# Kernel optimization log

Hardware: AMD Instinct MI355X
Metric: run time of the kernel (lower is better)

## Reference

```python
import jax, jax.numpy as jnp
import numpy as np

TEMP = 0.1
DX = 64  # feature dim of x; W1 rows [0:DX] multiply x, rows [DX:] multiply y


def setup_inputs() -> dict:
    key = jax.random.key(0)
    k1, k2, k3, k4 = jax.random.split(key, 4)
    n, d, hidden = 1024, 64, 256
    x = jax.random.normal(k1, (n, d), dtype=jnp.float32)
    y = jax.random.normal(k2, (n, d), dtype=jnp.float32)
    W1 = jax.random.normal(k3, (2 * d, hidden), dtype=jnp.float32) * (1.0 / np.sqrt(2 * d))
    b1 = jnp.zeros((hidden,), dtype=jnp.float32)
    w2 = jax.random.normal(k4, (hidden,), dtype=jnp.float32) * (1.0 / np.sqrt(hidden))
    b2 = jnp.zeros((), dtype=jnp.float32)
    return {"x": x, "y": y, "W1": W1, "b1": b1, "w2": w2, "b2": b2}


def reference(x, y, W1, b1, w2, b2):
    n = y.shape[0]
    W1x, W1y = W1[:DX], W1[DX:]
    xp = x @ W1x                      # [n, hidden], indexed by j (x_tile[i,j] = x[j])
    yp = y @ W1y                      # [n, hidden], indexed by i (y_tile[i,j] = y[i])
    # Positive pairs: scorer(cat(x_i, y_i))
    pos = (jax.nn.relu(xp + yp + b1) @ w2 + b2) / TEMP          # [n]
    h = jax.nn.relu(yp[:, None, :] + xp[None, :, :] + b1)        # [n, n, hidden]
    scores = (h @ w2 + b2) / TEMP                                 # [n, n]
    lse = jax.nn.logsumexp(scores, axis=1)                        # [n]
    lower_bound = pos.mean() - (lse.mean() - jnp.log(jnp.float32(n)))
    return -lower_bound
```

## Files before the change

### kernel.cpp

```cpp
#include <hip/hip_runtime.h>
#include <math.h>

#define NN 1024
#define DD 64
#define HH 256
#define TEMP_INV 10.0f
#define KCH 64
#define NCH (HH / KCH)


__global__ __launch_bounds__(256)
void k1_proj(const float* __restrict__ x, const float* __restrict__ y,
             const float* __restrict__ W1, const float* __restrict__ b1,
             float* __restrict__ xpbT, float* __restrict__ ypT)
{
    const int tid = threadIdx.x;
    const int i0 = blockIdx.x * 2;
    float ax0 = 0.f, ax1 = 0.f, ay0 = 0.f, ay1 = 0.f;
    #pragma unroll 8
    for (int kk = 0; kk < DD; ++kk) {
        const float wx = W1[kk * HH + tid];
        const float wy = W1[(DD + kk) * HH + tid];
        ax0 = fmaf(x[i0 * DD + kk],       wx, ax0);
        ax1 = fmaf(x[(i0 + 1) * DD + kk], wx, ax1);
        ay0 = fmaf(y[i0 * DD + kk],       wy, ay0);
        ay1 = fmaf(y[(i0 + 1) * DD + kk], wy, ay1);
    }
    const float b1t = b1[tid];
    *(float2*)&xpbT[tid * NN + i0] = make_float2(ax0 + b1t, ax1 + b1t);
    *(float2*)&ypT[tid * NN + i0]  = make_float2(ay0, ay1);
}

__global__ __launch_bounds__(512)
void k2_scores(const float* __restrict__ xpbT, const float* __restrict__ ypT,
               const float* __restrict__ w2, const float* __restrict__ b2,
               float* __restrict__ pmax, float* __restrict__ psum,
               float* __restrict__ pos)
{
    __shared__ float ys[2][KCH][64];
    __shared__ float xs[2][KCH][64];
    __shared__ float w2s[HH];
    const int t  = threadIdx.x;
    const int bj = blockIdx.x, bi = blockIdx.y;
    const int i0 = bi * 64, j0 = bj * 64;
    const int rr = t >> 5;
    const int cc = t & 31;

    if (t < HH) w2s[t] = w2[t];

    #define STAGE(c, buf)                                                      \
    {                                                                          \
        const int k0s = (c) * KCH;                                             \
        _Pragma("unroll")                                                      \
        for (int h = 0; h < 2; ++h) {                                          \
            const int f  = t + h * 512;                                        \
            const int r  = f >> 4;                                             \
            const int c4 = (f & 15) * 4;                                       \
            *(float4*)&ys[buf][r][c4] =                                        \
                *(const float4*)&ypT[(k0s + r) * NN + i0 + c4];                \
            *(float4*)&xs[buf][r][c4] =                                        \
                *(const float4*)&xpbT[(k0s + r) * NN + j0 + c4];               \
        }                                                                      \
    }

    float a00=0.f,a01=0.f, a10=0.f,a11=0.f, a20=0.f,a21=0.f, a30=0.f,a31=0.f;

    STAGE(0, 0);
    __syncthreads();
    for (int c = 0; c < NCH; ++c) {
        if (c + 1 < NCH) STAGE(c + 1, (c + 1) & 1);
        const int k0 = c * KCH;
        const int cur = c & 1;
        #pragma unroll 8
        for (int kk = 0; kk < KCH; ++kk) {
            const float w2k = w2s[k0 + kk];
            const float4 yv = *(const float4*)&ys[cur][kk][rr * 4];
            const float2 xv = *(const float2*)&xs[cur][kk][cc * 2];
            a00 = fmaf(fmaxf(yv.x + xv.x, 0.f), w2k, a00);
            a01 = fmaf(fmaxf(yv.x + xv.y, 0.f), w2k, a01);
            a10 = fmaf(fmaxf(yv.y + xv.x, 0.f), w2k, a10);
            a11 = fmaf(fmaxf(yv.y + xv.y, 0.f), w2k, a11);
            a20 = fmaf(fmaxf(yv.z + xv.x, 0.f), w2k, a20);
            a21 = fmaf(fmaxf(yv.z + xv.y, 0.f), w2k, a21);
            a30 = fmaf(fmaxf(yv.w + xv.x, 0.f), w2k, a30);
            a31 = fmaf(fmaxf(yv.w + xv.y, 0.f), w2k, a31);
        }
        __syncthreads();
    }
    #undef STAGE

    const float bb = b2[0];
    float s[4][2];
    s[0][0] = (a00 + bb) * TEMP_INV; s[0][1] = (a01 + bb) * TEMP_INV;
    s[1][0] = (a10 + bb) * TEMP_INV; s[1][1] = (a11 + bb) * TEMP_INV;
    s[2][0] = (a20 + bb) * TEMP_INV; s[2][1] = (a21 + bb) * TEMP_INV;
    s[3][0] = (a30 + bb) * TEMP_INV; s[3][1] = (a31 + bb) * TEMP_INV;

    if (bi == bj) {
        #pragma unroll
        for (int p = 0; p < 4; ++p)
            #pragma unroll
            for (int q = 0; q < 2; ++q)
                if (rr * 4 + p == cc * 2 + q)
                    pos[i0 + rr * 4 + p] = s[p][q];
    }

    float m[4], e[4];
    #pragma unroll
    for (int p = 0; p < 4; ++p) {
        m[p] = fmaxf(s[p][0], s[p][1]);
        e[p] = __expf(s[p][0] - m[p]) + __expf(s[p][1] - m[p]);
    }
    #pragma unroll
    for (int mk = 16; mk >= 1; mk >>= 1) {
        #pragma unroll
        for (int p = 0; p < 4; ++p) {
            const float mo = __shfl_xor(m[p], mk);
            const float eo = __shfl_xor(e[p], mk);
            const float mn = fmaxf(m[p], mo);
            e[p] = e[p] * __expf(m[p] - mn) + eo * __expf(mo - mn);
            m[p] = mn;
        }
    }
    if (cc == 0) {
        #pragma unroll
        for (int p = 0; p < 4; ++p) {
            const int row = i0 + rr * 4 + p;
            pmax[bj * NN + row] = m[p];
            psum[bj * NN + row] = e[p];
        }
    }
}

__global__ __launch_bounds__(1024)
void k3_final(const float* __restrict__ pmax, const float* __restrict__ psum,
              const float* __restrict__ pos, float* __restrict__ out)
{
    __shared__ float2 red[1024];
    const int tid = threadIdx.x;
    float M = pmax[tid], E = psum[tid];
    #pragma unroll
    for (int jc = 1; jc < 16; ++jc) {
        const float Mo = pmax[jc * NN + tid];
        const float Eo = psum[jc * NN + tid];
        const float Mn = fmaxf(M, Mo);
        E = E * __expf(M - Mn) + Eo * __expf(Mo - Mn);
        M = Mn;
    }
    red[tid] = make_float2(M + logf(E), pos[tid]);
    __syncthreads();
    for (int s = 512; s > 0; s >>= 1) {
        if (tid < s) {
            const float2 o = red[tid + s];
            float2 m2 = red[tid];
            m2.x += o.x; m2.y += o.y;
            red[tid] = m2;
        }
        __syncthreads();
    }
    if (tid == 0)
        out[0] = red[0].x / (float)NN - logf((float)NN) - red[0].y / (float)NN;
}

extern "C" void kernel_launch(void* const* d_in, const int* in_sizes, int n_in,
                              void* d_out, int out_size, void* d_ws, size_t ws_size,
                              hipStream_t stream)
{
    const float* x  = (const float*)d_in[0];
    const float* y  = (const float*)d_in[1];
    const float* W1 = (const float*)d_in[2];
    const float* b1 = (const float*)d_in[3];
    const float* w2 = (const float*)d_in[4];
    const float* b2 = (const float*)d_in[5];
    float* out = (float*)d_out;

    float* ws   = (float*)d_ws;
    float* xpbT = ws;
    float* ypT  = xpbT + HH * NN;
    float* pmax = ypT + HH * NN;
    float* psum = pmax + 16 * NN;
    float* pos  = psum + 16 * NN;

    hipLaunchKernelGGL(k1_proj, dim3(NN / 2), dim3(256), 0, stream,
                       x, y, W1, b1, xpbT, ypT);
    hipLaunchKernelGGL(k2_scores, dim3(16, 16), dim3(512), 0, stream,
                       xpbT, ypT, w2, b2, pmax, psum, pos);
    hipLaunchKernelGGL(k3_final, dim3(1), dim3(1024), 0, stream,
                       pmax, psum, pos, out);
}
```

Measured before the change: 41.26 us.

## Rewrite ReLU-weighted sum via |a+b| identity with sign-sorted hidden units

Uses relu(z)*w = 0.5*w*(z+|z|) and folds w2 into scaled projections, so the pairwise inner loop becomes sign*|y+x| accumulations. The linear part is precomputed as per-row sums A and B. Hidden units are reordered by sign of w2 (ballot/popcount) so each chunk uses a uniform sign, with a correction loop for the one chunk that straddles the boundary. The y operand is read directly from global memory in a row-major layout instead of being staged in LDS. This removes the per-element w2 multiply and LDS y reads, but adds scattered writes and reductions in k1. The uniform-sign fma relies on |w2| being folded into the projections, which holds only because w2 is scaled by 0.5*w2 and signs are handled separately.

```diff
diff --git a/kernel.cpp b/kernel.cpp
--- a/kernel.cpp
+++ b/kernel.cpp
@@ -6,14 +6,19 @@
 #define HH 256
 #define TEMP_INV 10.0f
 #define KCH 64
-#define NCH (HH / KCH)
+#define NCH 4
 
 
 __global__ __launch_bounds__(256)
 void k1_proj(const float* __restrict__ x, const float* __restrict__ y,
              const float* __restrict__ W1, const float* __restrict__ b1,
-             float* __restrict__ xpbT, float* __restrict__ ypT)
-{
+             const float* __restrict__ w2,
+             float* __restrict__ y2, float* __restrict__ x2T,
+             float* __restrict__ Aarr, float* __restrict__ Barr,
+             float* __restrict__ posr, int* __restrict__ kposD)
+{
+    __shared__ float red[6][256];
+    __shared__ unsigned int cnts[4];
     const int tid = threadIdx.x;
     const int i0 = blockIdx.x * 2;
     float ax0 = 0.f, ax1 = 0.f, ay0 = 0.f, ay1 = 0.f;
@@ -26,90 +31,132 @@
         ay0 = fmaf(y[i0 * DD + kk],       wy, ay0);
         ay1 = fmaf(y[(i0 + 1) * DD + kk], wy, ay1);
     }
-    const float b1t = b1[tid];
-    *(float2*)&xpbT[tid * NN + i0] = make_float2(ax0 + b1t, ax1 + b1t);
-    *(float2*)&ypT[tid * NN + i0]  = make_float2(ay0, ay1);
+    const float w2t = w2[tid], b1t = b1[tid];
+    const float xb0 = ax0 + b1t, xb1 = ax1 + b1t;
+    const float hw  = 0.5f * w2t;
+    const float xf0 = hw * xb0, xf1 = hw * xb1;
+    const float yf0 = hw * ay0, yf1 = hw * ay1;
+    const float p0 = fmaxf(ay0 + xb0, 0.f) * w2t;
+    const float p1 = fmaxf(ay1 + xb1, 0.f) * w2t;
+
+    const int lane = tid & 63, wv = tid >> 6;
+    const bool nonneg = (w2t >= 0.f);
+    const unsigned long long bal = __ballot(nonneg);
+    const int before = __popcll(bal & ((1ull << lane) - 1ull));
+    if (lane == 0) cnts[wv] = (unsigned int)__popcll(bal);
+    __syncthreads();
+    const int kpos = (int)(cnts[0] + cnts[1] + cnts[2] + cnts[3]);
+    int posbase = 0;
+    for (int u = 0; u < wv; ++u) posbase += (int)cnts[u];
+    const int rank = nonneg ? (posbase + before)
+                            : (kpos + wv * 64 - posbase + lane - before);
+
+    y2[(i0)     * HH + rank] = yf0;
+    y2[(i0 + 1) * HH + rank] = yf1;
+    *(float2*)&x2T[rank * NN + i0] = make_float2(xf0, xf1);
+    if (blockIdx.x == 0 && tid == 0) kposD[0] = kpos;
+
+    red[0][tid] = yf0; red[1][tid] = yf1;
+    red[2][tid] = xf0; red[3][tid] = xf1;
+    red[4][tid] = p0;  red[5][tid] = p1;
+    __syncthreads();
+    for (int s = 128; s > 0; s >>= 1) {
+        if (tid < s) {
+            #pragma unroll
+            for (int j = 0; j < 6; ++j) red[j][tid] += red[j][tid + s];
+        }
+        __syncthreads();
+    }
+    if (tid == 0) {
+        Aarr[i0] = red[0][0]; Aarr[i0 + 1] = red[1][0];
+        Barr[i0] = red[2][0]; Barr[i0 + 1] = red[3][0];
+        posr[i0] = red[4][0]; posr[i0 + 1] = red[5][0];
+    }
 }
 
 __global__ __launch_bounds__(512)
-void k2_scores(const float* __restrict__ xpbT, const float* __restrict__ ypT,
-               const float* __restrict__ w2, const float* __restrict__ b2,
-               float* __restrict__ pmax, float* __restrict__ psum,
-               float* __restrict__ pos)
-{
-    __shared__ float ys[2][KCH][64];
+void k2_scores(const float* __restrict__ x2T, const float* __restrict__ y2,
+               const float* __restrict__ Aarr, const float* __restrict__ Barr,
+               const float* __restrict__ b2, const int* __restrict__ kposD,
+               float* __restrict__ pmax, float* __restrict__ psum)
+{
     __shared__ float xs[2][KCH][64];
-    __shared__ float w2s[HH];
     const int t  = threadIdx.x;
     const int bj = blockIdx.x, bi = blockIdx.y;
     const int i0 = bi * 64, j0 = bj * 64;
     const int rr = t >> 5;
     const int cc = t & 31;
-
-    if (t < HH) w2s[t] = w2[t];
-
-    #define STAGE(c, buf)                                                      \
+    const int kpos = kposD[0];
+    const int rbase = i0 + rr * 4;
+
+    float acc[4][2];
+    #pragma unroll
+    for (int p = 0; p < 4; ++p) { acc[p][0] = 0.f; acc[p][1] = 0.f; }
+
+    #define STG(c, buf)                                                        \
     {                                                                          \
         const int k0s = (c) * KCH;                                             \
         _Pragma("unroll")                                                      \
         for (int h = 0; h < 2; ++h) {                                          \
-            const int f  = t + h * 512;                                        \
-            const int r  = f >> 4;                                             \
-            const int c4 = (f & 15) * 4;                                       \
-            *(float4*)&ys[buf][r][c4] =                                        \
-                *(const float4*)&ypT[(k0s + r) * NN + i0 + c4];                \
+            const int f = t + h * 512;                                         \
+            const int r = f >> 4, c4 = (f & 15) * 4;                           \
             *(float4*)&xs[buf][r][c4] =                                        \
-                *(const float4*)&xpbT[(k0s + r) * NN + j0 + c4];               \
+                *(const float4*)&x2T[(k0s + r) * NN + j0 + c4];                \
         }                                                                      \
     }
 
-    float a00=0.f,a01=0.f, a10=0.f,a11=0.f, a20=0.f,a21=0.f, a30=0.f,a31=0.f;
-
-    STAGE(0, 0);
+    STG(0, 0);
     __syncthreads();
     for (int c = 0; c < NCH; ++c) {
-        if (c + 1 < NCH) STAGE(c + 1, (c + 1) & 1);
+        if (c + 1 < NCH) STG(c + 1, (c + 1) & 1);
+        const int cur = c & 1;
         const int k0 = c * KCH;
-        const int cur = c & 1;
-        #pragma unroll 8
-        for (int kk = 0; kk < KCH; ++kk) {
-            const float w2k = w2s[k0 + kk];
-            const float4 yv = *(const float4*)&ys[cur][kk][rr * 4];
-            const float2 xv = *(const float2*)&xs[cur][kk][cc * 2];
-            a00 = fmaf(fmaxf(yv.x + xv.x, 0.f), w2k, a00);
-            a01 = fmaf(fmaxf(yv.x + xv.y, 0.f), w2k, a01);
-            a10 = fmaf(fmaxf(yv.y + xv.x, 0.f), w2k, a10);
-            a11 = fmaf(fmaxf(yv.y + xv.y, 0.f), w2k, a11);
-            a20 = fmaf(fmaxf(yv.z + xv.x, 0.f), w2k, a20);
-            a21 = fmaf(fmaxf(yv.z + xv.y, 0.f), w2k, a21);
-            a30 = fmaf(fmaxf(yv.w + xv.x, 0.f), w2k, a30);
-            a31 = fmaf(fmaxf(yv.w + xv.y, 0.f), w2k, a31);
+        const int mm = kpos - k0;
+        const float sgn = (mm > 0) ? 1.f : -1.f;
+        #pragma unroll 4
+        for (int g = 0; g < 16; ++g) {
+            const int kb = k0 + g * 4;
+            float4 yv[4];
+            #pragma unroll
+            for (int p = 0; p < 4; ++p)
+                yv[p] = *(const float4*)&y2[(rbase + p) * HH + kb];
+            #pragma unroll
+            for (int e = 0; e < 4; ++e) {
+                const float2 xv = *(const float2*)&xs[cur][g * 4 + e][cc * 2];
+                #pragma unroll
+                for (int p = 0; p < 4; ++p) {
+                    const float yp_ = (e == 0) ? yv[p].x : (e == 1) ? yv[p].y
+                                    : (e == 2) ? yv[p].z : yv[p].w;
+                    acc[p][0] = fmaf(sgn, fabsf(yp_ + xv.x), acc[p][0]);
+                    acc[p][1] = fmaf(sgn, fabsf(yp_ + xv.y), acc[p][1]);
+                }
+            }
+        }
+        if (mm > 0 && mm < KCH) {
+            for (int kk = mm; kk < KCH; ++kk) {
+                const float2 xv = *(const float2*)&xs[cur][kk][cc * 2];
+                #pragma unroll
+                for (int p = 0; p < 4; ++p) {
+                    const float yv1 = y2[(rbase + p) * HH + k0 + kk];
+                    acc[p][0] = fmaf(-2.f, fabsf(yv1 + xv.x), acc[p][0]);
+                    acc[p][1] = fmaf(-2.f, fabsf(yv1 + xv.y), acc[p][1]);
+                }
+            }
         }
         __syncthreads();
     }
-    #undef STAGE
+    #undef STG
 
     const float bb = b2[0];
-    float s[4][2];
-    s[0][0] = (a00 + bb) * TEMP_INV; s[0][1] = (a01 + bb) * TEMP_INV;
-    s[1][0] = (a10 + bb) * TEMP_INV; s[1][1] = (a11 + bb) * TEMP_INV;
-    s[2][0] = (a20 + bb) * TEMP_INV; s[2][1] = (a21 + bb) * TEMP_INV;
-    s[3][0] = (a30 + bb) * TEMP_INV; s[3][1] = (a31 + bb) * TEMP_INV;
-
-    if (bi == bj) {
-        #pragma unroll
-        for (int p = 0; p < 4; ++p)
-            #pragma unroll
-            for (int q = 0; q < 2; ++q)
-                if (rr * 4 + p == cc * 2 + q)
-                    pos[i0 + rr * 4 + p] = s[p][q];
-    }
-
+    const float Bv0 = Barr[j0 + cc * 2], Bv1 = Barr[j0 + cc * 2 + 1];
     float m[4], e[4];
     #pragma unroll
     for (int p = 0; p < 4; ++p) {
-        m[p] = fmaxf(s[p][0], s[p][1]);
-        e[p] = __expf(s[p][0] - m[p]) + __expf(s[p][1] - m[p]);
+        const float Av = Aarr[rbase + p];
+        const float s0 = (Av + Bv0 + acc[p][0] + bb) * TEMP_INV;
+        const float s1 = (Av + Bv1 + acc[p][1] + bb) * TEMP_INV;
+        m[p] = fmaxf(s0, s1);
+        e[p] = __expf(s0 - m[p]) + __expf(s1 - m[p]);
     }
     #pragma unroll
     for (int mk = 16; mk >= 1; mk >>= 1) {
@@ -125,19 +172,20 @@
     if (cc == 0) {
         #pragma unroll
         for (int p = 0; p < 4; ++p) {
-            const int row = i0 + rr * 4 + p;
-            pmax[bj * NN + row] = m[p];
-            psum[bj * NN + row] = e[p];
+            pmax[bj * NN + rbase + p] = m[p];
+            psum[bj * NN + rbase + p] = e[p];
         }
     }
 }
 
 __global__ __launch_bounds__(1024)
 void k3_final(const float* __restrict__ pmax, const float* __restrict__ psum,
-              const float* __restrict__ pos, float* __restrict__ out)
+              const float* __restrict__ posr, const float* __restrict__ b2,
+              float* __restrict__ out)
 {
     __shared__ float2 red[1024];
     const int tid = threadIdx.x;
+    const float bb = b2[0];
     float M = pmax[tid], E = psum[tid];
     #pragma unroll
     for (int jc = 1; jc < 16; ++jc) {
@@ -147,7 +195,8 @@
         E = E * __expf(M - Mn) + Eo * __expf(Mo - Mn);
         M = Mn;
     }
-    red[tid] = make_float2(M + logf(E), pos[tid]);
+    const float pos_s = (posr[tid] + bb) * TEMP_INV;
+    red[tid] = make_float2(M + logf(E), pos_s);
     __syncthreads();
     for (int s = 512; s > 0; s >>= 1) {
         if (tid < s) {
@@ -175,16 +224,19 @@
     float* out = (float*)d_out;
 
     float* ws   = (float*)d_ws;
-    float* xpbT = ws;
-    float* ypT  = xpbT + HH * NN;
-    float* pmax = ypT + HH * NN;
+    float* y2   = ws;
+    float* x2T  = y2 + NN * HH;
+    float* Aarr = x2T + HH * NN;
+    float* Barr = Aarr + NN;
+    float* posr = Barr + NN;
+    float* pmax = posr + NN;
     float* psum = pmax + 16 * NN;
-    float* pos  = psum + 16 * NN;
+    int*  kposD = (int*)(psum + 16 * NN);
 
     hipLaunchKernelGGL(k1_proj, dim3(NN / 2), dim3(256), 0, stream,
-                       x, y, W1, b1, xpbT, ypT);
+                       x, y, W1, b1, w2, y2, x2T, Aarr, Barr, posr, kposD);
     hipLaunchKernelGGL(k2_scores, dim3(16, 16), dim3(512), 0, stream,
-                       xpbT, ypT, w2, b2, pmax, psum, pos);
+                       x2T, y2, Aarr, Barr, b2, kposD, pmax, psum);
     hipLaunchKernelGGL(k3_final, dim3(1), dim3(1024), 0, stream,
-                       pmax, psum, pos, out);
-}
+                       pmax, psum, posr, b2, out);
+}
```

Result: slower. 45.20 us (+9.6%).

## Drop LDS staging in score kernel; read row-major y and use packed float2 math

Applied to the files above, without the earlier changes.

The y projection is now stored row-major so each thread loads its four rows as float4 vectors straight from global memory. The x projection is read directly from global memory, with no shared-memory double buffering and no __syncthreads. The inner ReLU-FMA loop uses 2-wide vector types so the compiler can emit packed FP32 instructions, and the grid becomes 16x32 blocks of 256 threads. This removes LDS traffic and barriers but relies on L1/L2 cache for data reuse, and each thread's y loads are strided across rows.

```diff
diff --git a/kernel.cpp b/kernel.cpp
--- a/kernel.cpp
+++ b/kernel.cpp
@@ -5,14 +5,14 @@
 #define DD 64
 #define HH 256
 #define TEMP_INV 10.0f
-#define KCH 64
-#define NCH (HH / KCH)
+
+typedef float v2f __attribute__((ext_vector_type(2)));
 
 
 __global__ __launch_bounds__(256)
 void k1_proj(const float* __restrict__ x, const float* __restrict__ y,
              const float* __restrict__ W1, const float* __restrict__ b1,
-             float* __restrict__ xpbT, float* __restrict__ ypT)
+             float* __restrict__ x2T, float* __restrict__ y2)
 {
     const int tid = threadIdx.x;
     const int i0 = blockIdx.x * 2;
@@ -27,89 +27,87 @@
         ay1 = fmaf(y[(i0 + 1) * DD + kk], wy, ay1);
     }
     const float b1t = b1[tid];
-    *(float2*)&xpbT[tid * NN + i0] = make_float2(ax0 + b1t, ax1 + b1t);
-    *(float2*)&ypT[tid * NN + i0]  = make_float2(ay0, ay1);
+    *(float2*)&x2T[tid * NN + i0] = make_float2(ax0 + b1t, ax1 + b1t);
+    y2[i0 * HH + tid]       = ay0;
+    y2[(i0 + 1) * HH + tid] = ay1;
 }
 
-__global__ __launch_bounds__(512)
-void k2_scores(const float* __restrict__ xpbT, const float* __restrict__ ypT,
+__global__ __launch_bounds__(256)
+void k2_scores(const float* __restrict__ x2T, const float* __restrict__ y2,
                const float* __restrict__ w2, const float* __restrict__ b2,
                float* __restrict__ pmax, float* __restrict__ psum,
                float* __restrict__ pos)
 {
-    __shared__ float ys[2][KCH][64];
-    __shared__ float xs[2][KCH][64];
-    __shared__ float w2s[HH];
     const int t  = threadIdx.x;
-    const int bj = blockIdx.x, bi = blockIdx.y;
-    const int i0 = bi * 64, j0 = bj * 64;
-    const int rr = t >> 5;
+    const int bj = blockIdx.x;
+    const int bi = blockIdx.y;
+    const int j0 = bj * 64;
+    const int rbase = bi * 32 + (t >> 5) * 4;
     const int cc = t & 31;
 
-    if (t < HH) w2s[t] = w2[t];
+    const float* yb = y2 + (size_t)rbase * HH;
+    const float* xb = x2T + j0 + cc * 2;
 
-    #define STAGE(c, buf)                                                      \
-    {                                                                          \
-        const int k0s = (c) * KCH;                                             \
-        _Pragma("unroll")                                                      \
-        for (int h = 0; h < 2; ++h) {                                          \
-            const int f  = t + h * 512;                                        \
-            const int r  = f >> 4;                                             \
-            const int c4 = (f & 15) * 4;                                       \
-            *(float4*)&ys[buf][r][c4] =                                        \
-                *(const float4*)&ypT[(k0s + r) * NN + i0 + c4];                \
-            *(float4*)&xs[buf][r][c4] =                                        \
-                *(const float4*)&xpbT[(k0s + r) * NN + j0 + c4];               \
-        }                                                                      \
+    v2f a0 = {0.f, 0.f}, a1 = {0.f, 0.f}, a2 = {0.f, 0.f}, a3 = {0.f, 0.f};
+    const v2f zero = {0.f, 0.f};
+
+    #pragma unroll 2
+    for (int g = 0; g < HH / 4; ++g) {
+        const int kb = g * 4;
+        const float4 yr0 = *(const float4*)&yb[kb];
+        const float4 yr1 = *(const float4*)&yb[HH + kb];
+        const float4 yr2 = *(const float4*)&yb[2 * HH + kb];
+        const float4 yr3 = *(const float4*)&yb[3 * HH + kb];
+        const v2f xv0 = *(const v2f*)&xb[(size_t)(kb + 0) * NN];
+        const v2f xv1 = *(const v2f*)&xb[(size_t)(kb + 1) * NN];
+        const v2f xv2 = *(const v2f*)&xb[(size_t)(kb + 2) * NN];
+        const v2f xv3 = *(const v2f*)&xb[(size_t)(kb + 3) * NN];
+#define STEP(XV, Y0, Y1, Y2, Y3, WK)                                          \
+        {                                                                     \
+            const float wk = (WK);                                            \
+            const v2f wv = {wk, wk};                                          \
+            v2f z;                                                            \
+            z = XV + (v2f){(Y0), (Y0)};                                       \
+            z = __builtin_elementwise_max(z, zero);                           \
+            a0 = z * wv + a0;                                                 \
+            z = XV + (v2f){(Y1), (Y1)};                                       \
+            z = __builtin_elementwise_max(z, zero);                           \
+            a1 = z * wv + a1;                                                 \
+            z = XV + (v2f){(Y2), (Y2)};                                       \
+            z = __builtin_elementwise_max(z, zero);                           \
+            a2 = z * wv + a2;                                                 \
+            z = XV + (v2f){(Y3), (Y3)};                                       \
+            z = __builtin_elementwise_max(z, zero);                           \
+            a3 = z * wv + a3;                                                 \
+        }
+        STEP(xv0, yr0.x, yr1.x, yr2.x, yr3.x, w2[kb + 0])
+        STEP(xv1, yr0.y, yr1.y, yr2.y, yr3.y, w2[kb + 1])
+        STEP(xv2, yr0.z, yr1.z, yr2.z, yr3.z, w2[kb + 2])
+        STEP(xv3, yr0.w, yr1.w, yr2.w, yr3.w, w2[kb + 3])
+#undef STEP
     }
 
-    float a00=0.f,a01=0.f, a10=0.f,a11=0.f, a20=0.f,a21=0.f, a30=0.f,a31=0.f;
+    const float bb = b2[0];
+    const v2f bbv = {bb, bb};
+    v2f sc[4];
+    sc[0] = (a0 + bbv) * TEMP_INV;
+    sc[1] = (a1 + bbv) * TEMP_INV;
+    sc[2] = (a2 + bbv) * TEMP_INV;
+    sc[3] = (a3 + bbv) * TEMP_INV;
 
-    STAGE(0, 0);
-    __syncthreads();
-    for (int c = 0; c < NCH; ++c) {
-        if (c + 1 < NCH) STAGE(c + 1, (c + 1) & 1);
-        const int k0 = c * KCH;
-        const int cur = c & 1;
-        #pragma unroll 8
-        for (int kk = 0; kk < KCH; ++kk) {
-            const float w2k = w2s[k0 + kk];
-            const float4 yv = *(const float4*)&ys[cur][kk][rr * 4];
-            const float2 xv = *(const float2*)&xs[cur][kk][cc * 2];
-            a00 = fmaf(fmaxf(yv.x + xv.x, 0.f), w2k, a00);
-            a01 = fmaf(fmaxf(yv.x + xv.y, 0.f), w2k, a01);
-            a10 = fmaf(fmaxf(yv.y + xv.x, 0.f), w2k, a10);
-            a11 = fmaf(fmaxf(yv.y + xv.y, 0.f), w2k, a11);
-            a20 = fmaf(fmaxf(yv.z + xv.x, 0.f), w2k, a20);
-            a21 = fmaf(fmaxf(yv.z + xv.y, 0.f), w2k, a21);
-            a30 = fmaf(fmaxf(yv.w + xv.x, 0.f), w2k, a30);
-            a31 = fmaf(fmaxf(yv.w + xv.y, 0.f), w2k, a31);
-        }
-        __syncthreads();
-    }
-    #undef STAGE
-
-    const float bb = b2[0];
-    float s[4][2];
-    s[0][0] = (a00 + bb) * TEMP_INV; s[0][1] = (a01 + bb) * TEMP_INV;
-    s[1][0] = (a10 + bb) * TEMP_INV; s[1][1] = (a11 + bb) * TEMP_INV;
-    s[2][0] = (a20 + bb) * TEMP_INV; s[2][1] = (a21 + bb) * TEMP_INV;
-    s[3][0] = (a30 + bb) * TEMP_INV; s[3][1] = (a31 + bb) * TEMP_INV;
-
-    if (bi == bj) {
-        #pragma unroll
-        for (int p = 0; p < 4; ++p)
-            #pragma unroll
-            for (int q = 0; q < 2; ++q)
-                if (rr * 4 + p == cc * 2 + q)
-                    pos[i0 + rr * 4 + p] = s[p][q];
+    const int col0 = j0 + cc * 2;
+    #pragma unroll
+    for (int p = 0; p < 4; ++p) {
+        const int row = rbase + p;
+        if (row == col0)     pos[row] = sc[p].x;
+        if (row == col0 + 1) pos[row] = sc[p].y;
     }
 
     float m[4], e[4];
     #pragma unroll
     for (int p = 0; p < 4; ++p) {
-        m[p] = fmaxf(s[p][0], s[p][1]);
-        e[p] = __expf(s[p][0] - m[p]) + __expf(s[p][1] - m[p]);
+        m[p] = fmaxf(sc[p].x, sc[p].y);
+        e[p] = __expf(sc[p].x - m[p]) + __expf(sc[p].y - m[p]);
     }
     #pragma unroll
     for (int mk = 16; mk >= 1; mk >>= 1) {
@@ -125,9 +123,8 @@
     if (cc == 0) {
         #pragma unroll
         for (int p = 0; p < 4; ++p) {
-            const int row = i0 + rr * 4 + p;
-            pmax[bj * NN + row] = m[p];
-            psum[bj * NN + row] = e[p];
+            pmax[bj * NN + rbase + p] = m[p];
+            psum[bj * NN + rbase + p] = e[p];
         }
     }
 }
@@ -175,16 +172,16 @@
     float* out = (float*)d_out;
 
     float* ws   = (float*)d_ws;
-    float* xpbT = ws;
-    float* ypT  = xpbT + HH * NN;
-    float* pmax = ypT + HH * NN;
+    float* x2T  = ws;
+    float* y2   = x2T + HH * NN;
+    float* pmax = y2 + NN * HH;
     float* psum = pmax + 16 * NN;
     float* pos  = psum + 16 * NN;
 
     hipLaunchKernelGGL(k1_proj, dim3(NN / 2), dim3(256), 0, stream,
-                       x, y, W1, b1, xpbT, ypT);
-    hipLaunchKernelGGL(k2_scores, dim3(16, 16), dim3(512), 0, stream,
-                       xpbT, ypT, w2, b2, pmax, psum, pos);
+                       x, y, W1, b1, x2T, y2);
+    hipLaunchKernelGGL(k2_scores, dim3(16, 32), dim3(256), 0, stream,
+                       x2T, y2, w2, b2, pmax, psum, pos);
     hipLaunchKernelGGL(k3_final, dim3(1), dim3(1024), 0, stream,
                        pmax, psum, pos, out);
 }
```

New measurement: 47.10 us. 1.14x slower.
